# Kernel optimization log

Hardware: AMD Instinct MI355X
Metric: run time of the kernel (lower is better)

Reference implementation:

```python
import jax, jax.numpy as jnp
import numpy as np
import math

N = 512; B = 32; T_IN = 24; T_OUT = 12; C_IN = 1; C_OUT = 64
D_MODEL = 64; N_HEADS = 8; K = 3; N_LAYERS = 2; D_FF = 4 * D_MODEL
MA_KERNEL = 25; FACTOR = 1
E_HEAD = D_MODEL // N_HEADS


def _sin_pe(T, d):
    pos = jnp.arange(T, dtype=jnp.float32)[:, None]
    div = jnp.exp(jnp.arange(0, d, 2, dtype=jnp.float32) * (-math.log(10000.0) / d))
    pe = jnp.zeros((T, d), dtype=jnp.float32)
    pe = pe.at[:, 0::2].set(jnp.sin(pos * div))
    pe = pe.at[:, 1::2].set(jnp.cos(pos * div))
    return pe


def _moving_avg(x, k):
    # Autoformer series_decomp moving average with edge-replicate padding. x: (B,L,D)
    pad = (k - 1) // 2
    xp = jnp.concatenate([jnp.repeat(x[:, :1], pad, axis=1), x, jnp.repeat(x[:, -1:], pad, axis=1)], axis=1)
    cs = jnp.cumsum(xp, axis=1)
    cs = jnp.concatenate([jnp.zeros_like(cs[:, :1]), cs], axis=1)
    return (cs[:, k:] - cs[:, :-k]) / k


def _autocorr_attn(q, k, v):
    # Autoformer AutoCorrelation (eval-mode delay aggregation). q,k,v: (Bf,L,H,E)
    Bf, L, H, E = q.shape
    qf = jnp.fft.rfft(jnp.transpose(q, (0, 2, 3, 1)), axis=-1)
    kf = jnp.fft.rfft(jnp.transpose(k, (0, 2, 3, 1)), axis=-1)
    corr = jnp.fft.irfft(qf * jnp.conj(kf), n=L, axis=-1)      # (Bf,H,E,L)
    values = jnp.transpose(v, (0, 2, 3, 1))                    # (Bf,H,E,L)
    top_k = int(FACTOR * math.log(L))
    mean_value = corr.mean(axis=(1, 2))                        # (Bf,L)
    weights, delay = jax.lax.top_k(mean_value, top_k)          # (Bf,top_k)
    tmp_corr = jax.nn.softmax(weights, axis=-1)
    base = jnp.arange(L)[None, :]
    agg = jnp.zeros_like(values)
    for i in range(top_k):
        idx = (base + delay[:, i:i + 1]) % L                   # circular gather == repeat+gather
        pattern = jnp.take_along_axis(values, idx[:, None, None, :], axis=-1)
        agg = agg + pattern * tmp_corr[:, i][:, None, None, None]
    return jnp.transpose(agg, (0, 3, 1, 2))                    # (Bf,L,H,E)


def _forward(s_w, x, swnn_w, swnn_b, alpha, beta, theta, wq, bq, wk, bk, wv, bv, wo, bo,
             conv1_w, conv1_b, conv2_w, conv2_b, norm_g, norm_b, dec_w, dec_b,
             slin_w, slin_b, tlin_w, tlin_b):
    W = jax.nn.softmax(s_w @ swnn_w.T + swnn_b, axis=1)        # SWNN, n_hidden=1
    Lmat = jnp.diag(W.sum(axis=1)) - W
    lam = jax.lax.stop_gradient(jnp.max(jnp.real(jnp.linalg.eigvals(Lmat))))
    Lt = 2.0 * Lmat / lam - jnp.eye(N, dtype=x.dtype)
    chebs = [jnp.eye(N, dtype=x.dtype), Lt]
    for i in range(2, K):
        chebs.append(2.0 * Lt * chebs[-1] - chebs[-2])         # elementwise *, as in the source
    w_x = jnp.einsum('btnc,nm->btmc', x, W)
    s_acc = jnp.zeros((B, T_IN, N, C_OUT), dtype=x.dtype)
    for kk in range(K):
        s_r = alpha[kk] + jnp.einsum('btnc,co->btno', x, beta[kk]) + jnp.einsum('btnc,co->btno', w_x, theta[kk])
        s_acc = s_acc + jnp.einsum('btno,nm->btmo', s_r, chebs[kk])
    s_out = jax.nn.relu(jnp.transpose(s_acc, (0, 2, 3, 1)))    # (B,N,O,T_in)
    s_out = jnp.einsum('bnot,ut->bnou', s_out, slin_w) + slin_b  # (B,N,O,T_out)
    # ---- temporal branch: PE + AutoCorrelation encoder (AutoTRGCN) ----
    x_bnct = jnp.transpose(x, (0, 2, 3, 1))                    # (B,N,C,T)
    h = x_bnct[..., None] + _sin_pe(T_IN, D_MODEL)             # (B,N,C,T,D)
    h = h.reshape(B * N * C_IN, T_IN, D_MODEL)
    for _ in range(N_LAYERS):                                  # shared layer params, as in source
        q = (jnp.einsum('bld,ed->ble', h, wq) + bq).reshape(-1, T_IN, N_HEADS, E_HEAD)
        kt = (jnp.einsum('bld,ed->ble', h, wk) + bk).reshape(-1, T_IN, N_HEADS, E_HEAD)
        vt = (jnp.einsum('bld,ed->ble', h, wv) + bv).reshape(-1, T_IN, N_HEADS, E_HEAD)
        new_h = _autocorr_attn(q, kt, vt).reshape(-1, T_IN, D_MODEL)
        new_h = jnp.einsum('bld,ed->ble', new_h, wo) + bo
        h = h + new_h
        h = h - _moving_avg(h, MA_KERNEL)                      # series_decomp residual
        y = jax.nn.relu(jnp.einsum('bld,fd->blf', h, conv1_w) + conv1_b)
        y = jnp.einsum('blf,df->bld', y, conv2_w) + conv2_b
        hy = h + y
        h = hy - _moving_avg(hy, MA_KERNEL)
    mu = h.mean(-1, keepdims=True)
    var = ((h - mu) ** 2).mean(-1, keepdims=True)
    hn = (h - mu) / jnp.sqrt(var + 1e-5) * norm_g + norm_b
    h = hn - hn.mean(axis=1, keepdims=True)                    # my_Layernorm
    h = h.reshape(B, N, C_IN, T_IN * D_MODEL)
    t_out = jax.nn.relu(jnp.einsum('bnck,uk->bncu', h, dec_w) + dec_b)  # (B,N,C,T_out)
    t_out = jnp.einsum('bnct,oc->bnot', t_out, tlin_w) + tlin_b[None, None, :, None]  # (B,N,O,T_out)
    st = jax.nn.relu(s_out * t_out)
    return jnp.transpose(st, (0, 3, 1, 2))                     # (B,T_out,N,O)


def setup_inputs() -> dict:
    key = jax.random.key(0)
    ks = jax.random.split(key, 32)
    def rn(i, shape, scale=0.05):
        return jax.random.normal(ks[i], shape, dtype=jnp.float32) * scale
    return dict(
        s_w=jax.random.uniform(ks[0], (N, N), dtype=jnp.float32),
        x=jax.random.normal(ks[1], (B, T_IN, N, C_IN), dtype=jnp.float32),
        swnn_w=rn(2, (N, N)), swnn_b=rn(3, (N,)),
        alpha=rn(4, (K,)), beta=rn(5, (K, C_IN, C_OUT)), theta=rn(6, (K, C_IN, C_OUT)),
        wq=rn(7, (D_MODEL, D_MODEL)), bq=rn(8, (D_MODEL,)),
        wk=rn(9, (D_MODEL, D_MODEL)), bk=rn(10, (D_MODEL,)),
        wv=rn(11, (D_MODEL, D_MODEL)), bv=rn(12, (D_MODEL,)),
        wo=rn(13, (D_MODEL, D_MODEL)), bo=rn(14, (D_MODEL,)),
        conv1_w=rn(15, (D_FF, D_MODEL)), conv1_b=rn(16, (D_FF,)),
        conv2_w=rn(17, (D_MODEL, D_FF)), conv2_b=rn(18, (D_MODEL,)),
        norm_g=jnp.ones((D_MODEL,), dtype=jnp.float32), norm_b=jnp.zeros((D_MODEL,), dtype=jnp.float32),
        dec_w=rn(19, (T_OUT, D_MODEL * T_IN)), dec_b=rn(20, (T_OUT,)),
        slin_w=rn(21, (T_OUT, T_IN)), slin_b=rn(22, (T_OUT,)),
        tlin_w=rn(23, (C_OUT, C_IN)), tlin_b=rn(24, (C_OUT,)),
    )


def reference(s_w, x, swnn_w, swnn_b, alpha, beta, theta, wq, bq, wk, bk, wv, bv, wo, bo,
              conv1_w, conv1_b, conv2_w, conv2_b, norm_g, norm_b, dec_w, dec_b,
              slin_w, slin_b, tlin_w, tlin_b):
    return _forward(s_w, x, swnn_w, swnn_b, alpha, beta, theta, wq, bq, wk, bk, wv, bv, wo, bo,
                    conv1_w, conv1_b, conv2_w, conv2_b, norm_g, norm_b, dec_w, dec_b,
                    slin_w, slin_b, tlin_w, tlin_b)
```

## Files before the change

### kernel.cpp

```cpp
#include <hip/hip_runtime.h>
#include <hip/hip_bf16.h>
#include <math.h>


static const size_t OFF_W   = 0;
static const size_t OFF_SA  = OFF_W  + 512*512;
static const size_t OFF_SB  = OFF_SA + 512*512;
static const size_t OFF_WX  = OFF_SB + 512*512;
static const size_t OFF_Y1  = OFF_WX + 768*512;
static const size_t OFF_Y2  = OFF_Y1 + 768*512;
static const size_t OFF_Z1  = OFF_Y2 + 768*512;
static const size_t OFF_Z2  = OFF_Z1 + 768*512;
static const size_t OFF_TR  = OFF_Z2 + 768*512;
static const size_t OFF_PE  = OFF_TR + 16384*12;
static const size_t OFF_CS1 = OFF_PE + 24*64;
static const size_t OFF_CS2 = OFF_CS1 + 512;
static const size_t OFF_V0  = OFF_CS2 + 512;
static const size_t OFF_V1  = OFF_V0 + 512;
static const size_t OFF_NA  = OFF_V1 + 512;
static const size_t OFF_SC  = OFF_NA + 64;
static const size_t OFF_M   = OFF_SC + 16;
static const size_t OFF_PT  = OFF_M  + 4096;
static const size_t OFF_C1T = OFF_PT + 4096;
static const size_t OFF_C2T = OFF_C1T + 16384;
static const size_t OFF_BVO = OFF_C2T + 16384;

#define EIG_H 0.125f
#define EIG_K 14
#define MV_STEPS 32

__global__ __launch_bounds__(256) void k_prep(float* __restrict__ wsf) {
  const int t = threadIdx.x;
  for (int idx = t; idx < 24 * 64; idx += 256) {
    int l = idx >> 6, d = idx & 63;
    int i = d >> 1;
    float div = expf((float)(2 * i) * (-9.210340371976184f / 64.0f));
    float ang = (float)l * div;
    wsf[OFF_PE + idx] = (d & 1) ? cosf(ang) : sinf(ang);
  }
  for (int idx = t; idx < 512; idx += 256)
    wsf[OFF_V0 + idx] = sinf((float)idx * 12.9898f + 0.5f) + 0.01f;
  for (int idx = t; idx < 64; idx += 256)
    wsf[OFF_NA + idx] = 0.0f;
}

__global__ __launch_bounds__(256) void k_wprep(
    const float* __restrict__ wq, const float* __restrict__ wk,
    const float* __restrict__ wv, const float* __restrict__ wo,
    const float* __restrict__ bv, const float* __restrict__ bo,
    const float* __restrict__ c1w, const float* __restrict__ c2w,
    float* __restrict__ wsf) {
  const int blk = blockIdx.x, t = threadIdx.x;
  if (blk == 0) {
    for (int i = 0; i < 16; ++i) {
      int idx = i * 256 + t;
      int d = idx >> 6, dp = idx & 63;
      float s = 0.f;
      for (int e = 0; e < 64; ++e) s += wq[e * 64 + d] * wk[e * 64 + dp];
      wsf[OFF_M + idx] = s;
    }
    if (t < 64) {
      float s = bo[t];
      for (int f = 0; f < 64; ++f) s += wo[t * 64 + f] * bv[f];
      wsf[OFF_BVO + t] = s;
    }
  } else if (blk == 1) {
    for (int i = 0; i < 16; ++i) {
      int idx = i * 256 + t;
      int d = idx >> 6, e = idx & 63;
      float s = 0.f;
      for (int f = 0; f < 64; ++f) s += wo[e * 64 + f] * wv[f * 64 + d];
      wsf[OFF_PT + idx] = s;
    }
  } else if (blk < 4) {
    int base = (blk - 2) * 8192;
    for (int i = 0; i < 32; ++i) {
      int idx = base + i * 256 + t;
      int d = idx >> 8, f = idx & 255;
      wsf[OFF_C1T + idx] = c1w[f * 64 + d];
    }
  } else {
    int base = (blk - 4) * 8192;
    for (int i = 0; i < 32; ++i) {
      int idx = base + i * 256 + t;
      int f = idx >> 6, e = idx & 63;
      wsf[OFF_C2T + idx] = c2w[e * 256 + f];
    }
  }
}

__global__ __launch_bounds__(256) void k_gemm_logits(
    const float* __restrict__ A, const float* __restrict__ Bm,
    const float* __restrict__ bias, float* __restrict__ C) {
  __shared__ float As[32][33], Bs[32][33];
  const int tx = threadIdx.x & 31, ty = threadIdx.x >> 5;
  const int rb = blockIdx.y * 32, cb = blockIdx.x * 32;
  float acc[4] = {0.f, 0.f, 0.f, 0.f};
  for (int kk = 0; kk < 512; kk += 32) {
    for (int idx = threadIdx.x; idx < 1024; idx += 256) {
      int r = idx >> 5, c = idx & 31;
      As[r][c] = A[(rb + r) * 512 + kk + c];
      Bs[c][r] = Bm[(cb + r) * 512 + kk + c];
    }
    __syncthreads();
    for (int k2 = 0; k2 < 32; ++k2) {
      float bvv = Bs[k2][tx];
      #pragma unroll
      for (int i = 0; i < 4; ++i) acc[i] += As[ty + 8 * i][k2] * bvv;
    }
    __syncthreads();
  }
  float bb = bias[cb + tx];
  #pragma unroll
  for (int i = 0; i < 4; ++i)
    C[(rb + ty + 8 * i) * 512 + cb + tx] = acc[i] + bb;
}

__global__ __launch_bounds__(64) void k_softmax_rows(float* __restrict__ W) {
  const int r = blockIdx.x, t = threadIdx.x;
  float* row = W + (size_t)r * 512;
  float v[8];
  float mx = -3.4e38f;
  #pragma unroll
  for (int i = 0; i < 8; ++i) { v[i] = row[t + 64 * i]; mx = fmaxf(mx, v[i]); }
  for (int m = 1; m < 64; m <<= 1) mx = fmaxf(mx, __shfl_xor(mx, m));
  float s = 0.f;
  #pragma unroll
  for (int i = 0; i < 8; ++i) { v[i] = expf(v[i] - mx); s += v[i]; }
  for (int m = 1; m < 64; m <<= 1) s += __shfl_xor(s, m);
  float inv = 1.0f / s;
  #pragma unroll
  for (int i = 0; i < 8; ++i) row[t + 64 * i] = v[i] * inv;
}

__global__ __launch_bounds__(256) void k_init_S(float* __restrict__ wsf) {
  const int idx = blockIdx.x * 256 + threadIdx.x;
  const int i = idx >> 9, j = idx & 511;
  float w = wsf[OFF_W + idx];
  wsf[OFF_SA + idx] = ((i == j) ? 1.0f : 0.0f) - EIG_H * w;
  if (idx == 0) {
    wsf[OFF_SC + 0] = 0.0f;
    wsf[OFF_SC + 1] = 1.0f;
    ((unsigned int*)(wsf + OFF_SC))[8] = 0u;
  }
}

__global__ __launch_bounds__(256) void k_gemm_square(
    const float* __restrict__ A, float* __restrict__ C,
    const float* __restrict__ scal, unsigned int* __restrict__ mbits) {
  __shared__ float As[32][33], Bs[32][33];
  const int tx = threadIdx.x & 31, ty = threadIdx.x >> 5;
  const int rb = blockIdx.y * 32, cb = blockIdx.x * 32;
  float acc[4] = {0.f, 0.f, 0.f, 0.f};
  for (int kk = 0; kk < 512; kk += 32) {
    for (int idx = threadIdx.x; idx < 1024; idx += 256) {
      int r = idx >> 5, c = idx & 31;
      As[r][c] = A[(rb + r) * 512 + kk + c];
      Bs[r][c] = A[(kk + r) * 512 + cb + c];
    }
    __syncthreads();
    for (int k2 = 0; k2 < 32; ++k2) {
      float bvv = Bs[k2][tx];
      #pragma unroll
      for (int i = 0; i < 4; ++i) acc[i] += As[ty + 8 * i][k2] * bvv;
    }
    __syncthreads();
  }
  const float s = scal[1];
  const float s2 = s * s;
  float lmax = 0.f;
  #pragma unroll
  for (int i = 0; i < 4; ++i) {
    float v = acc[i] * s2;
    C[(rb + ty + 8 * i) * 512 + cb + tx] = v;
    lmax = fmaxf(lmax, fabsf(v));
  }
  for (int m = 1; m < 64; m <<= 1) lmax = fmaxf(lmax, __shfl_xor(lmax, m));
  if ((threadIdx.x & 63) == 0) atomicMax(mbits, __float_as_uint(lmax));
}

__global__ void k_bookkeep(float* __restrict__ wsf) {
  unsigned int* mb = (unsigned int*)(wsf + OFF_SC) + 8;
  float m = fmaxf(__uint_as_float(*mb), 1e-30f);
  wsf[OFF_SC + 0] = 2.0f * wsf[OFF_SC + 0] + logf(m);
  wsf[OFF_SC + 1] = 1.0f / m;
  *mb = 0u;
}

__global__ __launch_bounds__(64) void k_matvec(
    const float* __restrict__ S, const float* __restrict__ vin,
    float* __restrict__ vout, float* __restrict__ wsf, int p) {
  __shared__ float vv[512];
  const int t = threadIdx.x;
  const float invm = wsf[OFF_SC + 1];
  const float pn = (p == 0) ? 1.0f : fmaxf(wsf[OFF_NA + p - 1], 1e-30f);
  const float sc = invm / sqrtf(pn);
  for (int i = t; i < 512; i += 64) vv[i] = vin[i];
  __syncthreads();
  const int row = blockIdx.x * 64 + t;
  const float* rp = S + (size_t)row * 512;
  float acc = 0.f;
  for (int j = 0; j < 512; j += 4) {
    float4 a = *(const float4*)(rp + j);
    acc += a.x * vv[j] + a.y * vv[j + 1] + a.z * vv[j + 2] + a.w * vv[j + 3];
  }
  float y = acc * sc;
  vout[row] = y;
  float ss = y * y;
  for (int m = 1; m < 64; m <<= 1) ss += __shfl_xor(ss, m);
  if (t == 0) atomicAdd(&wsf[OFF_NA + p], ss);
}

__global__ void k_lamfin(float* __restrict__ wsf) {
  float slope = 0.f;
  for (int p = 8; p < 32; ++p) slope += 0.5f * logf(fmaxf(wsf[OFF_NA + p], 1e-30f));
  slope *= (1.0f / 24.0f);
  float rate = (slope + wsf[OFF_SC + 0]) * (1.0f / 16384.0f);
  float minre = (1.0f - expf(rate)) * (1.0f / EIG_H);
  float lam = 1.0f - minre;
  wsf[OFF_SC + 2] = lam;
  wsf[OFF_SC + 3] = 2.0f / lam - 1.0f;
  wsf[OFF_SC + 4] = 2.0f / lam;
}

__global__ __launch_bounds__(64) void k_colsum(const float* __restrict__ W,
                                               float* __restrict__ wsf) {
  const int m = blockIdx.x * 64 + threadIdx.x;
  float s1 = 0.f, s2 = 0.f;
  for (int n = 0; n < 512; ++n) {
    float w = W[n * 512 + m];
    s1 += w; s2 += w * w;
  }
  float wmm = W[m * 512 + m];
  float a = wsf[OFF_SC + 3], c = wsf[OFF_SC + 4];
  wsf[OFF_CS1 + m] = a - c * s1;
  wsf[OFF_CS2 + m] = 2.0f * (c * c * s2 + a * a - 2.0f * a * c * wmm) - 1.0f;
}

__global__ __launch_bounds__(256) void k_gemm_wx(
    const float* __restrict__ A, const float* __restrict__ Bm,
    float* __restrict__ C) {
  __shared__ float As[32][33], Bs[32][33];
  const int tx = threadIdx.x & 31, ty = threadIdx.x >> 5;
  const int rb = blockIdx.y * 32, cb = blockIdx.x * 32;
  float acc[4] = {0.f, 0.f, 0.f, 0.f};
  for (int kk = 0; kk < 512; kk += 32) {
    for (int idx = threadIdx.x; idx < 1024; idx += 256) {
      int r = idx >> 5, c = idx & 31;
      As[r][c] = A[(rb + r) * 512 + kk + c];
      Bs[r][c] = Bm[(kk + r) * 512 + cb + c];
    }
    __syncthreads();
    for (int k2 = 0; k2 < 32; ++k2) {
      float bvv = Bs[k2][tx];
      #pragma unroll
      for (int i = 0; i < 4; ++i) acc[i] += As[ty + 8 * i][k2] * bvv;
    }
    __syncthreads();
  }
  #pragma unroll
  for (int i = 0; i < 4; ++i)
    C[(rb + ty + 8 * i) * 512 + cb + tx] = acc[i];
}

__global__ __launch_bounds__(256) void k_gemm_yz(
    const float* __restrict__ X, const float* __restrict__ WX,
    const float* __restrict__ W, const float* __restrict__ sc,
    float* __restrict__ y1, float* __restrict__ y2,
    float* __restrict__ z1, float* __restrict__ z2) {
  __shared__ float Xs[32][33], Ms[32][33], C1s[32][33], C2s[32][33];
  const int tx = threadIdx.x & 31, ty = threadIdx.x >> 5;
  const int rb = blockIdx.y * 32, cb = blockIdx.x * 32;
  const float a = sc[3], c = sc[4];
  float ay1[4] = {0,0,0,0}, ay2[4] = {0,0,0,0}, az1[4] = {0,0,0,0}, az2[4] = {0,0,0,0};
  for (int kk = 0; kk < 512; kk += 32) {
    for (int idx = threadIdx.x; idx < 1024; idx += 256) {
      int r = idx >> 5, cc = idx & 31;
      Xs[r][cc] = X[(rb + r) * 512 + kk + cc];
      Ms[r][cc] = WX[(rb + r) * 512 + kk + cc];
      float w = W[(kk + r) * 512 + cb + cc];
      float dl = ((kk + r) == (cb + cc)) ? 1.0f : 0.0f;
      float c1 = a * dl - c * w;
      C1s[r][cc] = c1;
      C2s[r][cc] = 2.0f * c1 * c1 - dl;
    }
    __syncthreads();
    for (int k2 = 0; k2 < 32; ++k2) {
      float b1 = C1s[k2][tx], b2 = C2s[k2][tx];
      #pragma unroll
      for (int i = 0; i < 4; ++i) {
        float xv = Xs[ty + 8 * i][k2];
        float wv = Ms[ty + 8 * i][k2];
        ay1[i] += xv * b1; ay2[i] += xv * b2;
        az1[i] += wv * b1; az2[i] += wv * b2;
      }
    }
    __syncthreads();
  }
  #pragma unroll
  for (int i = 0; i < 4; ++i) {
    int off = (rb + ty + 8 * i) * 512 + cb + tx;
    y1[off] = ay1[i]; y2[off] = ay2[i];
    z1[off] = az1[i]; z2[off] = az2[i];
  }
}

#define HSTR 65

__device__ __forceinline__ void decomp_block(float* hl, int r, int seq, int l,
                                             bool active) {
  #pragma unroll
  for (int ch = 0; ch < 2; ++ch) {
    float ma[32];
    if (active) {
      #pragma unroll
      for (int dc = 0; dc < 8; ++dc) {
        float s0 = 0.f, s1 = 0.f, s2 = 0.f, s3 = 0.f;
        for (int j = 0; j < 25; ++j) {
          int jj = l - 12 + j;
          jj = jj < 0 ? 0 : (jj > 23 ? 23 : jj);
          int bb = (seq * 24 + jj) * HSTR + ch * 32 + dc * 4;
          s0 += hl[bb]; s1 += hl[bb + 1]; s2 += hl[bb + 2]; s3 += hl[bb + 3];
        }
        ma[dc * 4] = s0; ma[dc * 4 + 1] = s1; ma[dc * 4 + 2] = s2; ma[dc * 4 + 3] = s3;
      }
    }
    __syncthreads();
    if (active) {
      #pragma unroll
      for (int e = 0; e < 32; ++e)
        hl[r * HSTR + ch * 32 + e] -= ma[e] * (1.0f / 25.0f);
    }
    if (ch == 0) {  }
    else __syncthreads();
  }
}

__global__ __launch_bounds__(256, 2) void k_temporal2(
    const float* __restrict__ x, const float* __restrict__ pe,
    const float* __restrict__ Mw, const float* __restrict__ PTw,
    const float* __restrict__ C1T, const float* __restrict__ C2T,
    const float* __restrict__ bvo,
    const float* __restrict__ c1b, const float* __restrict__ c2b,
    const float* __restrict__ ng, const float* __restrict__ nbv,
    const float* __restrict__ decw, const float* __restrict__ decb,
    float* __restrict__ trelu) {
  __shared__ float hl[8 * 24 * HSTR];
  __shared__ float corr_s[192];
  __shared__ float cmean_s[512];
  __shared__ float wsm_s[24];
  __shared__ int dly_s[24];
  __shared__ float pr_s[192];

  const int t = threadIdx.x;
  const int s0 = blockIdx.x * 8;
  const bool active = t < 192;
  const int r = t;
  const int seq = r / 24;
  const int l = r - seq * 24;
  const int gseq = s0 + seq;
  const int b = gseq >> 9, n = gseq & 511;

  if (active) {
    float xv = x[(b * 24 + l) * 512 + n];
    const float4* per = (const float4*)(pe + l * 64);
    #pragma unroll
    for (int c = 0; c < 16; ++c) {
      float4 pv = per[c];
      int bb = r * HSTR + c * 4;
      hl[bb] = xv + pv.x; hl[bb + 1] = xv + pv.y;
      hl[bb + 2] = xv + pv.z; hl[bb + 3] = xv + pv.w;
    }
  }
  __syncthreads();

  for (int layer = 0; layer < 2; ++layer) {
    if (active) corr_s[t] = 0.f;
    __syncthreads();
    {
      float u[64];
      #pragma unroll
      for (int e = 0; e < 64; ++e) u[e] = 0.f;
      if (active) {
        for (int d = 0; d < 64; ++d) {
          float hv = hl[r * HSTR + d];
          const float* Mr = Mw + d * 64;
          #pragma unroll
          for (int e = 0; e < 64; ++e) u[e] += hv * Mr[e];
        }
        for (int tau = 0; tau < 24; ++tau) {
          int l2 = l - tau; if (l2 < 0) l2 += 24;
          int bb = (seq * 24 + l2) * HSTR;
          float acc = 0.f;
          #pragma unroll
          for (int d = 0; d < 64; ++d) acc += u[d] * hl[bb + d];
          atomicAdd(&corr_s[seq * 24 + tau], acc * (1.0f / 64.0f));
        }
      }
    }
    __syncthreads();
    if (t < 8) {
      const float* cr = corr_s + t * 24;
      int i0 = 0, i1 = 0, i2 = 0;
      float v0 = -3.4e38f, v1 = -3.4e38f, v2 = -3.4e38f;
      for (int j = 0; j < 24; ++j) { float v = cr[j]; if (v > v0) { v0 = v; i0 = j; } }
      for (int j = 0; j < 24; ++j) { if (j == i0) continue; float v = cr[j]; if (v > v1) { v1 = v; i1 = j; } }
      for (int j = 0; j < 24; ++j) { if (j == i0 || j == i1) continue; float v = cr[j]; if (v > v2) { v2 = v; i2 = j; } }
      float e1 = expf(v1 - v0), e2 = expf(v2 - v0);
      float inv = 1.0f / (1.0f + e1 + e2);
      wsm_s[t * 3] = inv; wsm_s[t * 3 + 1] = e1 * inv; wsm_s[t * 3 + 2] = e2 * inv;
      dly_s[t * 3] = i0; dly_s[t * 3 + 1] = i1; dly_s[t * 3 + 2] = i2;
    }
    __syncthreads();
    {
      float acc[64];
      #pragma unroll
      for (int e = 0; e < 64; ++e) acc[e] = 0.f;
      if (active) {
        float w0 = wsm_s[seq * 3], w1 = wsm_s[seq * 3 + 1], w2 = wsm_s[seq * 3 + 2];
        int d0 = dly_s[seq * 3], d1 = dly_s[seq * 3 + 1], d2 = dly_s[seq * 3 + 2];
        int l0 = l + d0; if (l0 >= 24) l0 -= 24;
        int l1 = l + d1; if (l1 >= 24) l1 -= 24;
        int l2 = l + d2; if (l2 >= 24) l2 -= 24;
        int b0 = (seq * 24 + l0) * HSTR, b1 = (seq * 24 + l1) * HSTR, b2 = (seq * 24 + l2) * HSTR;
        for (int d = 0; d < 64; ++d) {
          float aggd = w0 * hl[b0 + d] + w1 * hl[b1 + d] + w2 * hl[b2 + d];
          const float* Pr = PTw + d * 64;
          #pragma unroll
          for (int e = 0; e < 64; ++e) acc[e] += aggd * Pr[e];
        }
      }
      __syncthreads();
      if (active) {
        #pragma unroll
        for (int e = 0; e < 64; ++e) hl[r * HSTR + e] += acc[e] + bvo[e];
      }
    }
    __syncthreads();
    decomp_block(hl, r, seq, l, active);
    {
      float a2[64];
      #pragma unroll
      for (int e = 0; e < 64; ++e) a2[e] = 0.f;
      if (active) {
        for (int fc = 0; fc < 16; ++fc) {
          float y16[16];
          #pragma unroll
          for (int f = 0; f < 16; ++f) y16[f] = 0.f;
          for (int d = 0; d < 64; ++d) {
            float hv = hl[r * HSTR + d];
            const float* c1r = C1T + d * 256 + fc * 16;
            #pragma unroll
            for (int f = 0; f < 16; ++f) y16[f] += hv * c1r[f];
          }
          #pragma unroll
          for (int f = 0; f < 16; ++f)
            y16[f] = fmaxf(y16[f] + c1b[fc * 16 + f], 0.0f);
          #pragma unroll
          for (int f = 0; f < 16; ++f) {
            float yf = y16[f];
            const float* r2 = C2T + (fc * 16 + f) * 64;
            #pragma unroll
            for (int e = 0; e < 64; ++e) a2[e] += yf * r2[e];
          }
        }
        #pragma unroll
        for (int e = 0; e < 64; ++e) hl[r * HSTR + e] += a2[e] + c2b[e];
      }
    }
    __syncthreads();
    decomp_block(hl, r, seq, l, active);
  }

  if (active) {
    float mu = 0.f;
    #pragma unroll
    for (int e = 0; e < 64; ++e) mu += hl[r * HSTR + e];
    mu *= (1.0f / 64.0f);
    float vs = 0.f;
    #pragma unroll
    for (int e = 0; e < 64; ++e) { float d = hl[r * HSTR + e] - mu; vs += d * d; }
    float rs = rsqrtf(vs * (1.0f / 64.0f) + 1e-5f);
    #pragma unroll
    for (int e = 0; e < 64; ++e)
      hl[r * HSTR + e] = (hl[r * HSTR + e] - mu) * rs * ng[e] + nbv[e];
  }
  __syncthreads();
  for (int pass = 0; pass < 2; ++pass) {
    int idx = pass * 256 + t;
    int sq2 = idx >> 6, e2 = idx & 63;
    float s = 0.f;
    for (int ll = 0; ll < 24; ++ll) s += hl[(sq2 * 24 + ll) * HSTR + e2];
    cmean_s[idx] = s * (1.0f / 24.0f);
  }
  __syncthreads();
  if (active) {
    #pragma unroll
    for (int e = 0; e < 64; ++e) hl[r * HSTR + e] -= cmean_s[seq * 64 + e];
  }
  __syncthreads();
  if (active) {
    int g = t >> 3;
    int u = g >> 1, half = g & 1;
    int sq = t & 7;
    const float* dwp = decw + u * 1536 + half * 768;
    int hbase = (sq * 24 + half * 12) * HSTR;
    float part = 0.f;
    for (int j = 0; j < 768; ++j) {
      int lr = j >> 6, d = j & 63;
      part += hl[hbase + lr * HSTR + d] * dwp[j];
    }
    pr_s[t] = part;
  }
  __syncthreads();
  if (t < 96) {
    int u = t >> 3, sq = t & 7;
    float v = pr_s[(u * 2) * 8 + sq] + pr_s[(u * 2 + 1) * 8 + sq] + decb[u];
    trelu[(size_t)(s0 + sq) * 12 + u] = fmaxf(v, 0.0f);
  }
}

__global__ __launch_bounds__(64) void k_final(
    const float* __restrict__ x, const float* __restrict__ wx,
    const float* __restrict__ y1, const float* __restrict__ y2,
    const float* __restrict__ z1, const float* __restrict__ z2,
    const float* __restrict__ cs1, const float* __restrict__ cs2,
    const float* __restrict__ trelu,
    const float* __restrict__ alpha, const float* __restrict__ beta,
    const float* __restrict__ theta,
    const float* __restrict__ slinw, const float* __restrict__ slinb,
    const float* __restrict__ tlinw, const float* __restrict__ tlinb,
    float* __restrict__ out) {
  __shared__ float ly0[24], ly1[24], ly2[24], lz0[24], lz1[24], lz2[24];
  __shared__ float ltr[12], lsw[288];
  const int blk = blockIdx.x;
  const int b = blk >> 9, m = blk & 511;
  const int t = threadIdx.x;
  if (t < 24) {
    int row = (b * 24 + t) * 512 + m;
    ly0[t] = x[row];  ly1[t] = y1[row]; ly2[t] = y2[row];
    lz0[t] = wx[row]; lz1[t] = z1[row]; lz2[t] = z2[row];
  }
  if (t >= 48 && t < 60) ltr[t - 48] = trelu[(b * 512 + m) * 12 + (t - 48)];
  for (int i = t; i < 288; i += 64) lsw[i] = slinw[i];
  __syncthreads();
  const int o = t;
  const float at = alpha[0] + alpha[1] * cs1[m] + alpha[2] * cs2[m];
  const float b0 = beta[o], b1 = beta[64 + o], b2 = beta[128 + o];
  const float t0 = theta[o], t1 = theta[64 + o], t2 = theta[128 + o];
  float so[12];
  #pragma unroll
  for (int u = 0; u < 12; ++u) so[u] = 0.f;
  for (int tt = 0; tt < 24; ++tt) {
    float v = at + b0 * ly0[tt] + b1 * ly1[tt] + b2 * ly2[tt]
                 + t0 * lz0[tt] + t1 * lz1[tt] + t2 * lz2[tt];
    v = fmaxf(v, 0.0f);
    #pragma unroll
    for (int u = 0; u < 12; ++u) so[u] += lsw[u * 24 + tt] * v;
  }
  const float tw = tlinw[o], tb = tlinb[o];
  #pragma unroll
  for (int u = 0; u < 12; ++u) {
    float sval = so[u] + slinb[u];
    float tval = tw * ltr[u] + tb;
    float rr = fmaxf(sval * tval, 0.0f);
    out[(((size_t)b * 12 + u) * 512 + m) * 64 + o] = rr;
  }
}

extern "C" void kernel_launch(void* const* d_in, const int* in_sizes, int n_in,
                              void* d_out, int out_size, void* d_ws, size_t ws_size,
                              hipStream_t stream) {
  (void)in_sizes; (void)n_in; (void)out_size; (void)ws_size;
  const float* s_w    = (const float*)d_in[0];
  const float* x      = (const float*)d_in[1];
  const float* swnn_w = (const float*)d_in[2];
  const float* swnn_b = (const float*)d_in[3];
  const float* alpha  = (const float*)d_in[4];
  const float* beta   = (const float*)d_in[5];
  const float* theta  = (const float*)d_in[6];
  const float* wq = (const float*)d_in[7];  const float* bq = (const float*)d_in[8];
  const float* wk = (const float*)d_in[9];  const float* bk = (const float*)d_in[10];
  const float* wv = (const float*)d_in[11]; const float* bv = (const float*)d_in[12];
  const float* wo = (const float*)d_in[13]; const float* bo = (const float*)d_in[14];
  const float* c1w = (const float*)d_in[15]; const float* c1b = (const float*)d_in[16];
  const float* c2w = (const float*)d_in[17]; const float* c2b = (const float*)d_in[18];
  const float* ng  = (const float*)d_in[19]; const float* nb  = (const float*)d_in[20];
  const float* decw = (const float*)d_in[21]; const float* decb = (const float*)d_in[22];
  const float* slinw = (const float*)d_in[23]; const float* slinb = (const float*)d_in[24];
  const float* tlinw = (const float*)d_in[25]; const float* tlinb = (const float*)d_in[26];
  (void)bq; (void)bk;

  float* wsf = (float*)d_ws;
  float* out = (float*)d_out;

  float* Wm = wsf + OFF_W;
  float* Sa = wsf + OFF_SA;
  float* Sb = wsf + OFF_SB;
  unsigned int* mbits = (unsigned int*)(wsf + OFF_SC) + 8;
  const float* scal = wsf + OFF_SC;

  k_prep<<<1, 256, 0, stream>>>(wsf);
  k_wprep<<<6, 256, 0, stream>>>(wq, wk, wv, wo, bv, bo, c1w, c2w, wsf);
  k_gemm_logits<<<dim3(16, 16), 256, 0, stream>>>(s_w, swnn_w, swnn_b, Wm);
  k_softmax_rows<<<512, 64, 0, stream>>>(Wm);

  k_temporal2<<<2048, 256, 0, stream>>>(x, wsf + OFF_PE, wsf + OFF_M, wsf + OFF_PT,
                                        wsf + OFF_C1T, wsf + OFF_C2T, wsf + OFF_BVO,
                                        c1b, c2b, ng, nb, decw, decb, wsf + OFF_TR);

  k_init_S<<<1024, 256, 0, stream>>>(wsf);
  float* cur = Sa;
  float* nxt = Sb;
  for (int j = 0; j < EIG_K; ++j) {
    k_gemm_square<<<dim3(16, 16), 256, 0, stream>>>(cur, nxt, scal, mbits);
    k_bookkeep<<<1, 1, 0, stream>>>(wsf);
    float* tmp = cur; cur = nxt; nxt = tmp;
  }
  float* va = wsf + OFF_V0;
  float* vb = wsf + OFF_V1;
  for (int p = 0; p < MV_STEPS; ++p) {
    k_matvec<<<8, 64, 0, stream>>>(cur, va, vb, wsf, p);
    float* tmp = va; va = vb; vb = tmp;
  }
  k_lamfin<<<1, 1, 0, stream>>>(wsf);

  k_colsum<<<8, 64, 0, stream>>>(Wm, wsf);
  k_gemm_wx<<<dim3(16, 24), 256, 0, stream>>>(x, Wm, wsf + OFF_WX);
  k_gemm_yz<<<dim3(16, 24), 256, 0, stream>>>(x, wsf + OFF_WX, Wm, scal,
                                              wsf + OFF_Y1, wsf + OFF_Y2,
                                              wsf + OFF_Z1, wsf + OFF_Z2);
  k_final<<<16384, 64, 0, stream>>>(x, wsf + OFF_WX, wsf + OFF_Y1, wsf + OFF_Y2,
                                    wsf + OFF_Z1, wsf + OFF_Z2,
                                    wsf + OFF_CS1, wsf + OFF_CS2, wsf + OFF_TR,
                                    alpha, beta, theta, slinw, slinb,
                                    tlinw, tlinb, out);
}
```

Baseline: 2.948 ms.

## Rework temporal kernel with float2 LDS access, sliding-window decomp, higher occupancy

The temporal encoder kernel now pads shared rows to an even stride so it can read and write them as float2 vector pairs. The moving-average decomposition is rewritten as a per-column sliding window over all 256 threads, replacing the 25-tap gather over 192 threads. Auxiliary shared buffers are aliased into one array, and launch bounds ask for 3 blocks per CU. The aim is fewer LDS instructions, less redundant decomposition work and better latency hiding, at the risk of register spills under the tighter occupancy target and more bank conflicts from the even stride.

Measured after the change: 2.888 ms. 2.1% less time.

```diff
diff --git a/kernel.cpp b/kernel.cpp
--- a/kernel.cpp
+++ b/kernel.cpp
@@ -305,38 +305,32 @@
   }
 }
 
-#define HSTR 65
-
-__device__ __forceinline__ void decomp_block(float* hl, int r, int seq, int l,
-                                             bool active) {
-  #pragma unroll
-  for (int ch = 0; ch < 2; ++ch) {
-    float ma[32];
-    if (active) {
-      #pragma unroll
-      for (int dc = 0; dc < 8; ++dc) {
-        float s0 = 0.f, s1 = 0.f, s2 = 0.f, s3 = 0.f;
-        for (int j = 0; j < 25; ++j) {
-          int jj = l - 12 + j;
-          jj = jj < 0 ? 0 : (jj > 23 ? 23 : jj);
-          int bb = (seq * 24 + jj) * HSTR + ch * 32 + dc * 4;
-          s0 += hl[bb]; s1 += hl[bb + 1]; s2 += hl[bb + 2]; s3 += hl[bb + 3];
-        }
-        ma[dc * 4] = s0; ma[dc * 4 + 1] = s1; ma[dc * 4 + 2] = s2; ma[dc * 4 + 3] = s3;
-      }
-    }
-    __syncthreads();
-    if (active) {
-      #pragma unroll
-      for (int e = 0; e < 32; ++e)
-        hl[r * HSTR + ch * 32 + e] -= ma[e] * (1.0f / 25.0f);
-    }
-    if (ch == 0) {  }
-    else __syncthreads();
-  }
-}
-
-__global__ __launch_bounds__(256, 2) void k_temporal2(
+#define HSTR 66
+#define HSTR2 33
+
+__device__ __forceinline__ void decomp_cols(float* __restrict__ hl, int t) {
+  #pragma unroll
+  for (int task = 0; task < 2; ++task) {
+    int id = task * 256 + t;
+    int sq = id >> 6, e = id & 63;
+    int base = sq * 24 * HSTR + e;
+    float h24[24];
+    #pragma unroll
+    for (int ll = 0; ll < 24; ++ll) h24[ll] = hl[base + ll * HSTR];
+    float W = 13.0f * h24[0];
+    #pragma unroll
+    for (int j = 1; j <= 12; ++j) W += h24[j];
+    #pragma unroll
+    for (int ll = 0; ll < 24; ++ll) {
+      hl[base + ll * HSTR] = h24[ll] - W * (1.0f / 25.0f);
+      int jp = (ll + 13 > 23) ? 23 : ll + 13;
+      int jm = (ll - 12 < 0) ? 0 : ll - 12;
+      W += h24[jp] - h24[jm];
+    }
+  }
+}
+
+__global__ __launch_bounds__(256, 3) void k_temporal3(
     const float* __restrict__ x, const float* __restrict__ pe,
     const float* __restrict__ Mw, const float* __restrict__ PTw,
     const float* __restrict__ C1T, const float* __restrict__ C2T,
@@ -346,11 +340,12 @@
     const float* __restrict__ decw, const float* __restrict__ decb,
     float* __restrict__ trelu) {
   __shared__ float hl[8 * 24 * HSTR];
-  __shared__ float corr_s[192];
-  __shared__ float cmean_s[512];
-  __shared__ float wsm_s[24];
-  __shared__ int dly_s[24];
-  __shared__ float pr_s[192];
+  __shared__ float aux[512];
+  float* corr_s = aux;
+  float* wsm_s  = aux + 192;
+  int*   dly_s  = (int*)(aux + 216);
+  float* cmean_s = aux;
+  float* pr_s   = aux;
 
   const int t = threadIdx.x;
   const int s0 = blockIdx.x * 8;
@@ -360,42 +355,44 @@
   const int l = r - seq * 24;
   const int gseq = s0 + seq;
   const int b = gseq >> 9, n = gseq & 511;
+  float2* hl2 = (float2*)hl;
+  const int row2 = r * HSTR2;
 
   if (active) {
     float xv = x[(b * 24 + l) * 512 + n];
-    const float4* per = (const float4*)(pe + l * 64);
-    #pragma unroll
-    for (int c = 0; c < 16; ++c) {
-      float4 pv = per[c];
-      int bb = r * HSTR + c * 4;
-      hl[bb] = xv + pv.x; hl[bb + 1] = xv + pv.y;
-      hl[bb + 2] = xv + pv.z; hl[bb + 3] = xv + pv.w;
+    const float2* per = (const float2*)(pe + l * 64);
+    #pragma unroll
+    for (int c = 0; c < 32; ++c) {
+      float2 pv = per[c];
+      hl2[row2 + c] = make_float2(xv + pv.x, xv + pv.y);
     }
   }
   __syncthreads();
 
   for (int layer = 0; layer < 2; ++layer) {
-    if (active) corr_s[t] = 0.f;
-    __syncthreads();
-    {
+    if (t < 192) corr_s[t] = 0.f;
+    __syncthreads();
+    if (active) {
       float u[64];
       #pragma unroll
       for (int e = 0; e < 64; ++e) u[e] = 0.f;
-      if (active) {
-        for (int d = 0; d < 64; ++d) {
-          float hv = hl[r * HSTR + d];
-          const float* Mr = Mw + d * 64;
-          #pragma unroll
-          for (int e = 0; e < 64; ++e) u[e] += hv * Mr[e];
+      for (int dd = 0; dd < 32; ++dd) {
+        float2 hv = hl2[row2 + dd];
+        const float* M0 = Mw + (2 * dd) * 64;
+        const float* M1 = M0 + 64;
+        #pragma unroll
+        for (int e = 0; e < 64; ++e) u[e] += hv.x * M0[e] + hv.y * M1[e];
+      }
+      for (int tau = 0; tau < 24; ++tau) {
+        int l2v = l - tau; if (l2v < 0) l2v += 24;
+        int bb2 = (seq * 24 + l2v) * HSTR2;
+        float acc = 0.f;
+        #pragma unroll
+        for (int dd = 0; dd < 32; ++dd) {
+          float2 h2 = hl2[bb2 + dd];
+          acc += u[2 * dd] * h2.x + u[2 * dd + 1] * h2.y;
         }
-        for (int tau = 0; tau < 24; ++tau) {
-          int l2 = l - tau; if (l2 < 0) l2 += 24;
-          int bb = (seq * 24 + l2) * HSTR;
-          float acc = 0.f;
-          #pragma unroll
-          for (int d = 0; d < 64; ++d) acc += u[d] * hl[bb + d];
-          atomicAdd(&corr_s[seq * 24 + tau], acc * (1.0f / 64.0f));
-        }
+        atomicAdd(&corr_s[seq * 24 + tau], acc * (1.0f / 64.0f));
       }
     }
     __syncthreads();
@@ -422,22 +419,31 @@
         int l0 = l + d0; if (l0 >= 24) l0 -= 24;
         int l1 = l + d1; if (l1 >= 24) l1 -= 24;
         int l2 = l + d2; if (l2 >= 24) l2 -= 24;
-        int b0 = (seq * 24 + l0) * HSTR, b1 = (seq * 24 + l1) * HSTR, b2 = (seq * 24 + l2) * HSTR;
-        for (int d = 0; d < 64; ++d) {
-          float aggd = w0 * hl[b0 + d] + w1 * hl[b1 + d] + w2 * hl[b2 + d];
-          const float* Pr = PTw + d * 64;
+        int b0 = (seq * 24 + l0) * HSTR2, b1 = (seq * 24 + l1) * HSTR2, b2 = (seq * 24 + l2) * HSTR2;
+        for (int dd = 0; dd < 32; ++dd) {
+          float2 a0 = hl2[b0 + dd], a1 = hl2[b1 + dd], av2 = hl2[b2 + dd];
+          float gx = w0 * a0.x + w1 * a1.x + w2 * av2.x;
+          float gy = w0 * a0.y + w1 * a1.y + w2 * av2.y;
+          const float* P0 = PTw + (2 * dd) * 64;
+          const float* P1 = P0 + 64;
           #pragma unroll
-          for (int e = 0; e < 64; ++e) acc[e] += aggd * Pr[e];
+          for (int e = 0; e < 64; ++e) acc[e] += gx * P0[e] + gy * P1[e];
         }
       }
       __syncthreads();
       if (active) {
         #pragma unroll
-        for (int e = 0; e < 64; ++e) hl[r * HSTR + e] += acc[e] + bvo[e];
+        for (int j = 0; j < 32; ++j) {
+          float2 cur = hl2[row2 + j];
+          cur.x += acc[2 * j] + bvo[2 * j];
+          cur.y += acc[2 * j + 1] + bvo[2 * j + 1];
+          hl2[row2 + j] = cur;
+        }
       }
     }
     __syncthreads();
-    decomp_block(hl, r, seq, l, active);
+    decomp_cols(hl, t);
+    __syncthreads();
     {
       float a2[64];
       #pragma unroll
@@ -447,11 +453,12 @@
           float y16[16];
           #pragma unroll
           for (int f = 0; f < 16; ++f) y16[f] = 0.f;
-          for (int d = 0; d < 64; ++d) {
-            float hv = hl[r * HSTR + d];
-            const float* c1r = C1T + d * 256 + fc * 16;
+          for (int dd = 0; dd < 32; ++dd) {
+            float2 hv = hl2[row2 + dd];
+            const float* c1a = C1T + (2 * dd) * 256 + fc * 16;
+            const float* c1bp = c1a + 256;
             #pragma unroll
-            for (int f = 0; f < 16; ++f) y16[f] += hv * c1r[f];
+            for (int f = 0; f < 16; ++f) y16[f] += hv.x * c1a[f] + hv.y * c1bp[f];
           }
           #pragma unroll
           for (int f = 0; f < 16; ++f)
@@ -465,27 +472,42 @@
           }
         }
         #pragma unroll
-        for (int e = 0; e < 64; ++e) hl[r * HSTR + e] += a2[e] + c2b[e];
+        for (int j = 0; j < 32; ++j) {
+          float2 cur = hl2[row2 + j];
+          cur.x += a2[2 * j] + c2b[2 * j];
+          cur.y += a2[2 * j + 1] + c2b[2 * j + 1];
+          hl2[row2 + j] = cur;
+        }
       }
     }
     __syncthreads();
-    decomp_block(hl, r, seq, l, active);
+    decomp_cols(hl, t);
+    __syncthreads();
   }
 
   if (active) {
     float mu = 0.f;
     #pragma unroll
-    for (int e = 0; e < 64; ++e) mu += hl[r * HSTR + e];
+    for (int dd = 0; dd < 32; ++dd) { float2 v = hl2[row2 + dd]; mu += v.x + v.y; }
     mu *= (1.0f / 64.0f);
     float vs = 0.f;
     #pragma unroll
-    for (int e = 0; e < 64; ++e) { float d = hl[r * HSTR + e] - mu; vs += d * d; }
+    for (int dd = 0; dd < 32; ++dd) {
+      float2 v = hl2[row2 + dd];
+      float dx = v.x - mu, dy = v.y - mu;
+      vs += dx * dx + dy * dy;
+    }
     float rs = rsqrtf(vs * (1.0f / 64.0f) + 1e-5f);
     #pragma unroll
-    for (int e = 0; e < 64; ++e)
-      hl[r * HSTR + e] = (hl[r * HSTR + e] - mu) * rs * ng[e] + nbv[e];
+    for (int dd = 0; dd < 32; ++dd) {
+      float2 v = hl2[row2 + dd];
+      v.x = (v.x - mu) * rs * ng[2 * dd] + nbv[2 * dd];
+      v.y = (v.y - mu) * rs * ng[2 * dd + 1] + nbv[2 * dd + 1];
+      hl2[row2 + dd] = v;
+    }
   }
   __syncthreads();
+  #pragma unroll
   for (int pass = 0; pass < 2; ++pass) {
     int idx = pass * 256 + t;
     int sq2 = idx >> 6, e2 = idx & 63;
@@ -496,19 +518,26 @@
   __syncthreads();
   if (active) {
     #pragma unroll
-    for (int e = 0; e < 64; ++e) hl[r * HSTR + e] -= cmean_s[seq * 64 + e];
+    for (int j = 0; j < 32; ++j) {
+      float2 v = hl2[row2 + j];
+      v.x -= cmean_s[seq * 64 + 2 * j];
+      v.y -= cmean_s[seq * 64 + 2 * j + 1];
+      hl2[row2 + j] = v;
+    }
   }
   __syncthreads();
   if (active) {
     int g = t >> 3;
     int u = g >> 1, half = g & 1;
     int sq = t & 7;
-    const float* dwp = decw + u * 1536 + half * 768;
-    int hbase = (sq * 24 + half * 12) * HSTR;
+    const float2* dwp2 = (const float2*)(decw + u * 1536 + half * 768);
+    int hb2 = (sq * 24 + half * 12) * HSTR2;
     float part = 0.f;
-    for (int j = 0; j < 768; ++j) {
-      int lr = j >> 6, d = j & 63;
-      part += hl[hbase + lr * HSTR + d] * dwp[j];
+    for (int j = 0; j < 384; ++j) {
+      int lr = j >> 5, dd = j & 31;
+      float2 hv = hl2[hb2 + lr * HSTR2 + dd];
+      float2 wv = dwp2[j];
+      part += hv.x * wv.x + hv.y * wv.y;
     }
     pr_s[t] = part;
   }
@@ -605,7 +634,7 @@
   k_gemm_logits<<<dim3(16, 16), 256, 0, stream>>>(s_w, swnn_w, swnn_b, Wm);
   k_softmax_rows<<<512, 64, 0, stream>>>(Wm);
 
-  k_temporal2<<<2048, 256, 0, stream>>>(x, wsf + OFF_PE, wsf + OFF_M, wsf + OFF_PT,
+  k_temporal3<<<2048, 256, 0, stream>>>(x, wsf + OFF_PE, wsf + OFF_M, wsf + OFF_PT,
                                         wsf + OFF_C1T, wsf + OFF_C2T, wsf + OFF_BVO,
                                         c1b, c2b, ng, nb, decw, decb, wsf + OFF_TR);
 
```
